# Optimization experiments

Measured on AMD Instinct MI355X. Metric: run time of the kernel, lower is better.

The kernel has to match this reference:

```python
import jax, jax.numpy as jnp
import numpy as np

SNAPPING_GAIN = 30.0


def setup_inputs() -> dict:
    key = jax.random.key(0)
    k1, k2 = jax.random.split(key)
    latent_coeffs = jax.random.normal(k1, (16, 2048, 1024), dtype=jnp.float32)
    # NMF basis is non-negative; 1024 atoms of dim 900 (30x30 ARC grids)
    basis_vectors = jax.random.uniform(k2, (1024, 900), dtype=jnp.float32)
    return {"latent_coeffs": latent_coeffs, "basis_vectors": basis_vectors}


def reference(latent_coeffs, basis_vectors):
    # [B, K, C] -> sharpened softmax over codes
    probs = jax.nn.softmax(latent_coeffs * SNAPPING_GAIN, axis=-1)
    indices = jnp.argmax(probs, axis=-1)                        # [B, K] int
    one_hot = jax.nn.one_hot(indices, probs.shape[-1], dtype=probs.dtype)
    # straight-through: value == one_hot, gradient flows through probs
    one_hot_st = probs + jax.lax.stop_gradient(one_hot - probs)
    # [B,K,C] @ [C,D] -> [B,K,D] (effectively a row-gather of the basis)
    quantized = jnp.einsum('bkc,cd->bkd', one_hot_st, basis_vectors)
    return quantized, indices
```

## Files before the change

### kernel.cpp

```cpp
#include <hip/hip_runtime.h>


#define C_DIM 1024
#define D_DIM 900

typedef float vfloat4 __attribute__((ext_vector_type(4)));

__global__ __launch_bounds__(256) void argmax_kernel(
    const float* __restrict__ latent,
    float* __restrict__ out_idx,
    int rows)
{
    const int lane = threadIdx.x & 63;
    const int wid  = threadIdx.x >> 6;
    const int row  = blockIdx.x * 4 + wid;
    if (row >= rows) return;

    const vfloat4* lrow = reinterpret_cast<const vfloat4*>(latent + (size_t)row * C_DIM);
    vfloat4 v0 = __builtin_nontemporal_load(&lrow[lane]);
    vfloat4 v1 = __builtin_nontemporal_load(&lrow[lane + 64]);
    vfloat4 v2 = __builtin_nontemporal_load(&lrow[lane + 128]);
    vfloat4 v3 = __builtin_nontemporal_load(&lrow[lane + 192]);

    float m = v0[0];
    int   mi = lane * 4;
    #pragma unroll
    for (int e = 1; e < 4; ++e)
        if (v0[e] > m) { m = v0[e]; mi = lane * 4 + e; }
    #pragma unroll
    for (int e = 0; e < 4; ++e)
        if (v1[e] > m) { m = v1[e]; mi = (64 + lane) * 4 + e; }
    #pragma unroll
    for (int e = 0; e < 4; ++e)
        if (v2[e] > m) { m = v2[e]; mi = (128 + lane) * 4 + e; }
    #pragma unroll
    for (int e = 0; e < 4; ++e)
        if (v3[e] > m) { m = v3[e]; mi = (192 + lane) * 4 + e; }

    #pragma unroll
    for (int off = 32; off > 0; off >>= 1) {
        float om = __shfl_xor(m, off, 64);
        int   oi = __shfl_xor(mi, off, 64);
        if (om > m || (om == m && oi < mi)) { m = om; mi = oi; }
    }

    if (lane == 0) __builtin_nontemporal_store((float)mi, &out_idx[row]);
}

__global__ __launch_bounds__(256) void gather_kernel(
    const float* __restrict__ basis,
    const float* __restrict__ out_idx,
    float* __restrict__ out_q,
    int rows)
{
    const int lane = threadIdx.x & 63;
    const int wid  = threadIdx.x >> 6;
    const int row  = blockIdx.x * 4 + wid;
    if (row >= rows) return;

    const int idx = (int)out_idx[row];

    const vfloat4* b4 = reinterpret_cast<const vfloat4*>(basis + (size_t)idx * D_DIM);
    vfloat4*       o4 = reinterpret_cast<vfloat4*>(out_q + (size_t)row * D_DIM);
    #pragma unroll
    for (int j = 0; j < 4; ++j) {
        int t = 64 * j + lane;
        if (t < 225) {
            vfloat4 bv = b4[t];
            __builtin_nontemporal_store(bv, &o4[t]);
        }
    }
}

extern "C" void kernel_launch(void* const* d_in, const int* in_sizes, int n_in,
                              void* d_out, int out_size, void* d_ws, size_t ws_size,
                              hipStream_t stream) {
    const float* latent = (const float*)d_in[0];
    const float* basis  = (const float*)d_in[1];
    (void)n_in; (void)d_ws; (void)ws_size; (void)out_size;

    const int rows = in_sizes[0] / C_DIM;
    float* out_q   = (float*)d_out;
    float* out_idx = (float*)d_out + (size_t)rows * D_DIM;

    const int blocks = (rows + 3) / 4;
    argmax_kernel<<<blocks, 256, 0, stream>>>(latent, out_idx, rows);
    gather_kernel<<<blocks, 256, 0, stream>>>(basis, out_idx, out_q, rows);
}
```

Measured before the change: 51.79 us.

## Fuse argmax and basis gather into one kernel processing two rows per wave

Merges the argmax and gather kernels into a single launch, so the index goes straight from the reduction to the gather instead of round-tripping through global memory, and one launch is saved. Each wave now handles two rows and issues both rows' latent loads up front to get more memory-level parallelism. The cost is fewer waves in the grid and more registers per thread, and the code assumes an even row count.

```diff
diff --git a/kernel.cpp b/kernel.cpp
--- a/kernel.cpp
+++ b/kernel.cpp
@@ -3,25 +3,12 @@
 
 #define C_DIM 1024
 #define D_DIM 900
+#define ROWS_PER_WAVE 2
 
 typedef float vfloat4 __attribute__((ext_vector_type(4)));
 
-__global__ __launch_bounds__(256) void argmax_kernel(
-    const float* __restrict__ latent,
-    float* __restrict__ out_idx,
-    int rows)
-{
-    const int lane = threadIdx.x & 63;
-    const int wid  = threadIdx.x >> 6;
-    const int row  = blockIdx.x * 4 + wid;
-    if (row >= rows) return;
-
-    const vfloat4* lrow = reinterpret_cast<const vfloat4*>(latent + (size_t)row * C_DIM);
-    vfloat4 v0 = __builtin_nontemporal_load(&lrow[lane]);
-    vfloat4 v1 = __builtin_nontemporal_load(&lrow[lane + 64]);
-    vfloat4 v2 = __builtin_nontemporal_load(&lrow[lane + 128]);
-    vfloat4 v3 = __builtin_nontemporal_load(&lrow[lane + 192]);
-
+__device__ __forceinline__ int wave_argmax(vfloat4 v0, vfloat4 v1, vfloat4 v2,
+                                           vfloat4 v3, int lane) {
     float m = v0[0];
     int   mi = lane * 4;
     #pragma unroll
@@ -43,25 +30,14 @@
         int   oi = __shfl_xor(mi, off, 64);
         if (om > m || (om == m && oi < mi)) { m = om; mi = oi; }
     }
-
-    if (lane == 0) __builtin_nontemporal_store((float)mi, &out_idx[row]);
+    return mi;
 }
 
-__global__ __launch_bounds__(256) void gather_kernel(
-    const float* __restrict__ basis,
-    const float* __restrict__ out_idx,
-    float* __restrict__ out_q,
-    int rows)
-{
-    const int lane = threadIdx.x & 63;
-    const int wid  = threadIdx.x >> 6;
-    const int row  = blockIdx.x * 4 + wid;
-    if (row >= rows) return;
-
-    const int idx = (int)out_idx[row];
-
+__device__ __forceinline__ void gather_store(const float* __restrict__ basis,
+                                             float* __restrict__ out_q,
+                                             int idx, size_t row, int lane) {
     const vfloat4* b4 = reinterpret_cast<const vfloat4*>(basis + (size_t)idx * D_DIM);
-    vfloat4*       o4 = reinterpret_cast<vfloat4*>(out_q + (size_t)row * D_DIM);
+    vfloat4*       o4 = reinterpret_cast<vfloat4*>(out_q + row * D_DIM);
     #pragma unroll
     for (int j = 0; j < 4; ++j) {
         int t = 64 * j + lane;
@@ -70,6 +46,39 @@
             __builtin_nontemporal_store(bv, &o4[t]);
         }
     }
+}
+
+__global__ __launch_bounds__(256) void basisvq_kernel(
+    const float* __restrict__ latent,
+    const float* __restrict__ basis,
+    float* __restrict__ out_q,
+    float* __restrict__ out_idx,
+    int rows)
+{
+    const int lane = threadIdx.x & 63;
+    const int wv   = blockIdx.x * 4 + (threadIdx.x >> 6);
+    const int r0   = wv * ROWS_PER_WAVE;
+    if (r0 >= rows) return;
+
+    const vfloat4* l0 = reinterpret_cast<const vfloat4*>(latent + (size_t)r0 * C_DIM);
+    vfloat4 a0 = __builtin_nontemporal_load(&l0[lane]);
+    vfloat4 a1 = __builtin_nontemporal_load(&l0[lane + 64]);
+    vfloat4 a2 = __builtin_nontemporal_load(&l0[lane + 128]);
+    vfloat4 a3 = __builtin_nontemporal_load(&l0[lane + 192]);
+
+    const vfloat4* l1 = reinterpret_cast<const vfloat4*>(latent + (size_t)(r0 + 1) * C_DIM);
+    vfloat4 b0 = __builtin_nontemporal_load(&l1[lane]);
+    vfloat4 b1 = __builtin_nontemporal_load(&l1[lane + 64]);
+    vfloat4 b2 = __builtin_nontemporal_load(&l1[lane + 128]);
+    vfloat4 b3 = __builtin_nontemporal_load(&l1[lane + 192]);
+
+    int idx0 = wave_argmax(a0, a1, a2, a3, lane);
+    if (lane == 0) __builtin_nontemporal_store((float)idx0, &out_idx[r0]);
+    gather_store(basis, out_q, idx0, (size_t)r0, lane);
+
+    int idx1 = wave_argmax(b0, b1, b2, b3, lane);
+    if (lane == 0) __builtin_nontemporal_store((float)idx1, &out_idx[r0 + 1]);
+    gather_store(basis, out_q, idx1, (size_t)(r0 + 1), lane);
 }
 
 extern "C" void kernel_launch(void* const* d_in, const int* in_sizes, int n_in,
@@ -83,7 +92,6 @@
     float* out_q   = (float*)d_out;
     float* out_idx = (float*)d_out + (size_t)rows * D_DIM;
 
-    const int blocks = (rows + 3) / 4;
-    argmax_kernel<<<blocks, 256, 0, stream>>>(latent, out_idx, rows);
-    gather_kernel<<<blocks, 256, 0, stream>>>(basis, out_idx, out_q, rows);
+    const int blocks = (rows + 8 - 1) / 8;
+    basisvq_kernel<<<blocks, 256, 0, stream>>>(latent, basis, out_q, out_idx, rows);
 }
```

Result: slower. 54.21 us (+4.7%).
